# Optimization experiments

Hardware: AMD Instinct MI355X
Metric: run time of the kernel (lower is better)

The kernel has to match this reference:

```python
import jax, jax.numpy as jnp
import numpy as np

N = 4096  # square [B, T+1] as required by original indexing (T = shape[0], indexed on dim 1)
GAMMA = 0.99

def setup_inputs() -> dict:
    key = jax.random.key(0)
    ks = jax.random.split(key, 6)
    shape = (N, N)
    names = ["Q", "expected_target_Q", "target_Q", "rewards",
             "target_policy_probs", "behaviour_policy_probs"]
    return {n: jax.random.normal(k, shape, dtype=jnp.float32) for n, k in zip(names, ks)}

def _retrace_loss(Q, expected_target_Q, target_Q, rewards,
                  target_policy_probs, behaviour_policy_probs):
    rewards = rewards * 100.0
    # retrace weights c_t = exp(min(log pi - log b, 0)) = min(1, pi/b)
    c_ret = jnp.exp(jnp.minimum(target_policy_probs - behaviour_policy_probs, 0.0))
    T = Q.shape[0]  # faithful to original (square inputs => equals time length)
    last = target_Q[:, T - 1]  # Q_ret[:, -1] = target_Q[:, -1]
    # reverse-time linear recurrence via a single scan:
    # Q_ret[t-1] = r[t-1] + gamma*c[t]*(Q_ret[t] - target_Q[t]) + gamma*E[t]
    xs = (rewards[:, :T - 1].T[::-1],          # [T-1, B], t-1 = T-2 .. 0
          c_ret[:, 1:T].T[::-1],               # c[t],  t = T-1 .. 1
          target_Q[:, 1:T].T[::-1],
          expected_target_Q[:, 1:T].T[::-1])

    def step(q_next, x):
        r, c, tq, eq = x
        q = r + GAMMA * c * (q_next - tq) + GAMMA * eq
        return q, q

    _, qs = jax.lax.scan(step, last, xs)       # qs: [T-1, B] for t = T-2 .. 0
    Q_ret = jnp.concatenate([qs[::-1].T, last[:, None]], axis=1)  # [B, T]
    Q_ret = jax.lax.stop_gradient(Q_ret)       # computed under torch.no_grad()
    return jnp.mean((Q - Q_ret) ** 2)

def reference(Q, expected_target_Q, target_Q, rewards,
              target_policy_probs, behaviour_policy_probs):
    return _retrace_loss(Q, expected_target_Q, target_Q, rewards,
                         target_policy_probs, behaviour_policy_probs)
```

## Files before the change

### kernel.cpp

```cpp
#include <hip/hip_runtime.h>


#define NROWS 4096
#define TLEN  4096
#define BLOCK 256
#define EPT   16

__global__ __launch_bounds__(BLOCK) void retrace_main(
    const float* __restrict__ Q,
    const float* __restrict__ eQ,
    const float* __restrict__ tQ,
    const float* __restrict__ rw,
    const float* __restrict__ tpp,
    const float* __restrict__ bpp,
    double* __restrict__ partials)
{
    constexpr float G = 0.99f;
    __shared__ float sA[BLOCK];
    __shared__ float sB[BLOCK];
    __shared__ float sRed[BLOCK / 64];

    const int tid = threadIdx.x;
    const long long base = (long long)blockIdx.x * TLEN;
    const int ua = (TLEN - EPT) - EPT * tid;

    float Aa[17], Bb[17];

    float prev_r = 0.0f;
    #pragma unroll
    for (int g = 0; g < 4; ++g) {
        const float4 r4 = *(const float4*)(rw  + base + ua + 4 * g);
        const float4 t4 = *(const float4*)(tpp + base + ua + 4 * g);
        const float4 p4 = *(const float4*)(bpp + base + ua + 4 * g);
        const float4 q4 = *(const float4*)(tQ  + base + ua + 4 * g);
        const float4 e4 = *(const float4*)(eQ  + base + ua + 4 * g);
        const float rv[4] = {r4.x, r4.y, r4.z, r4.w};
        const float tv[4] = {t4.x, t4.y, t4.z, t4.w};
        const float pv[4] = {p4.x, p4.y, p4.z, p4.w};
        const float qv[4] = {q4.x, q4.y, q4.z, q4.w};
        const float ev[4] = {e4.x, e4.y, e4.z, e4.w};
        #pragma unroll
        for (int e = 0; e < 4; ++e) {
            const int m = 4 * g + e;
            if (m >= 1) {
                const float c  = __expf(fminf(tv[e] - pv[e], 0.0f));
                const float gc = G * c;
                const float f  = fmaf(-gc, qv[e], G * ev[e]);
                const float rp = (e == 0) ? prev_r : rv[e - 1];
                Aa[m] = gc;
                Bb[m] = fmaf(100.0f, rp, f);
            }
        }
        prev_r = rv[3];
    }
    if (tid == 0) {
        Aa[16] = 0.0f;
        Bb[16] = tQ[base + TLEN - 1];
    } else {
        const float tx = tpp[base + ua + 16];
        const float px = bpp[base + ua + 16];
        const float qx = tQ [base + ua + 16];
        const float ex = eQ [base + ua + 16];
        const float c  = __expf(fminf(tx - px, 0.0f));
        const float gc = G * c;
        const float f  = fmaf(-gc, qx, G * ex);
        Aa[16] = gc;
        Bb[16] = fmaf(100.0f, prev_r, f);
    }

    float Ac = 1.0f, Bc = 0.0f;
    #pragma unroll
    for (int k = 0; k < EPT; ++k) {
        const int m = 16 - k;
        Bc = fmaf(Aa[m], Bc, Bb[m]);
        Ac = Aa[m] * Ac;
    }

    sA[tid] = Ac; sB[tid] = Bc;
    __syncthreads();
    #pragma unroll
    for (int off = 1; off < BLOCK; off <<= 1) {
        float a1 = 0.0f, b1 = 0.0f;
        const bool has = (tid >= off);
        if (has) { a1 = sA[tid - off]; b1 = sB[tid - off]; }
        const float a2 = sA[tid], b2 = sB[tid];
        __syncthreads();
        if (has) { sA[tid] = a2 * a1; sB[tid] = fmaf(a2, b1, b2); }
        __syncthreads();
    }
    float y = (tid == 0) ? 0.0f : sB[tid - 1];

    float qq[16];
    #pragma unroll
    for (int g = 0; g < 4; ++g) {
        const float4 Q4 = *(const float4*)(Q + base + ua + 4 * g);
        qq[4 * g + 0] = Q4.x; qq[4 * g + 1] = Q4.y;
        qq[4 * g + 2] = Q4.z; qq[4 * g + 3] = Q4.w;
    }
    float acc = 0.0f;
    #pragma unroll
    for (int k = 0; k < EPT; ++k) {
        const int m = 16 - k;
        y = fmaf(Aa[m], y, Bb[m]);
        const float d = qq[m - 1] - y;
        acc = fmaf(d, d, acc);
    }

    #pragma unroll
    for (int off = 32; off > 0; off >>= 1)
        acc += __shfl_down(acc, off, 64);
    if ((tid & 63) == 0) sRed[tid >> 6] = acc;
    __syncthreads();
    if (tid == 0) {
        const float s = sRed[0] + sRed[1] + sRed[2] + sRed[3];
        partials[blockIdx.x] = (double)s;
    }
}

__global__ __launch_bounds__(BLOCK) void retrace_finalize(
    const double* __restrict__ partials, float* __restrict__ out)
{
    __shared__ double sRed[BLOCK / 64];
    double s = 0.0;
    for (int i = threadIdx.x; i < NROWS; i += BLOCK) s += partials[i];
    #pragma unroll
    for (int off = 32; off > 0; off >>= 1)
        s += __shfl_down(s, off, 64);
    if ((threadIdx.x & 63) == 0) sRed[threadIdx.x >> 6] = s;
    __syncthreads();
    if (threadIdx.x == 0) {
        const double tot = sRed[0] + sRed[1] + sRed[2] + sRed[3];
        out[0] = (float)(tot / ((double)NROWS * (double)TLEN));
    }
}

extern "C" void kernel_launch(void* const* d_in, const int* in_sizes, int n_in,
                              void* d_out, int out_size, void* d_ws, size_t ws_size,
                              hipStream_t stream)
{
    const float* Q   = (const float*)d_in[0];
    const float* eQ  = (const float*)d_in[1];
    const float* tQ  = (const float*)d_in[2];
    const float* rw  = (const float*)d_in[3];
    const float* tpp = (const float*)d_in[4];
    const float* bpp = (const float*)d_in[5];
    double* partials = (double*)d_ws;

    retrace_main<<<NROWS, BLOCK, 0, stream>>>(Q, eQ, tQ, rw, tpp, bpp, partials);
    retrace_finalize<<<1, BLOCK, 0, stream>>>(partials, (float*)d_out);
}
```

Baseline: 345.1 us.

## Replace shared-memory block scan with wavefront shuffle scan and hoist all loads

```diff
diff --git a/kernel.cpp b/kernel.cpp
--- a/kernel.cpp
+++ b/kernel.cpp
@@ -16,100 +16,120 @@
     double* __restrict__ partials)
 {
     constexpr float G = 0.99f;
-    __shared__ float sA[BLOCK];
-    __shared__ float sB[BLOCK];
-    __shared__ float sRed[BLOCK / 64];
+    __shared__ float sWA[4], sWB[4];
+    __shared__ float sRed[4];
 
-    const int tid = threadIdx.x;
+    const int tid  = threadIdx.x;
+    const int lane = tid & 63;
+    const int wv   = tid >> 6;
     const long long base = (long long)blockIdx.x * TLEN;
     const int ua = (TLEN - EPT) - EPT * tid;
 
-    float Aa[17], Bb[17];
+    float4 Rv4[4], Tv4[4], Pv4[4], Qt4[4], Ev4[4], Qm4[4];
+    #pragma unroll
+    for (int g = 0; g < 4; ++g) Rv4[g] = *(const float4*)(rw  + base + ua + 4 * g);
+    #pragma unroll
+    for (int g = 0; g < 4; ++g) Tv4[g] = *(const float4*)(tpp + base + ua + 4 * g);
+    #pragma unroll
+    for (int g = 0; g < 4; ++g) Pv4[g] = *(const float4*)(bpp + base + ua + 4 * g);
+    #pragma unroll
+    for (int g = 0; g < 4; ++g) Qt4[g] = *(const float4*)(tQ  + base + ua + 4 * g);
+    #pragma unroll
+    for (int g = 0; g < 4; ++g) Ev4[g] = *(const float4*)(eQ  + base + ua + 4 * g);
+    #pragma unroll
+    for (int g = 0; g < 4; ++g) Qm4[g] = *(const float4*)(Q   + base + ua + 4 * g);
 
-    float prev_r = 0.0f;
+    const bool bnd = (lane == 0) && (tid != 0);
+    float bt = 0.f, bp = 0.f, bq = 0.f, be = 0.f;
+    if (bnd) {
+        bt = tpp[base + ua + 16];
+        bp = bpp[base + ua + 16];
+        bq = tQ [base + ua + 16];
+        be = eQ [base + ua + 16];
+    }
+
+    float rv[16], tv[16], pv[16], qv[16], ev[16], qm[16];
     #pragma unroll
     for (int g = 0; g < 4; ++g) {
-        const float4 r4 = *(const float4*)(rw  + base + ua + 4 * g);
-        const float4 t4 = *(const float4*)(tpp + base + ua + 4 * g);
-        const float4 p4 = *(const float4*)(bpp + base + ua + 4 * g);
-        const float4 q4 = *(const float4*)(tQ  + base + ua + 4 * g);
-        const float4 e4 = *(const float4*)(eQ  + base + ua + 4 * g);
-        const float rv[4] = {r4.x, r4.y, r4.z, r4.w};
-        const float tv[4] = {t4.x, t4.y, t4.z, t4.w};
-        const float pv[4] = {p4.x, p4.y, p4.z, p4.w};
-        const float qv[4] = {q4.x, q4.y, q4.z, q4.w};
-        const float ev[4] = {e4.x, e4.y, e4.z, e4.w};
-        #pragma unroll
-        for (int e = 0; e < 4; ++e) {
-            const int m = 4 * g + e;
-            if (m >= 1) {
-                const float c  = __expf(fminf(tv[e] - pv[e], 0.0f));
-                const float gc = G * c;
-                const float f  = fmaf(-gc, qv[e], G * ev[e]);
-                const float rp = (e == 0) ? prev_r : rv[e - 1];
-                Aa[m] = gc;
-                Bb[m] = fmaf(100.0f, rp, f);
-            }
+        rv[4*g+0]=Rv4[g].x; rv[4*g+1]=Rv4[g].y; rv[4*g+2]=Rv4[g].z; rv[4*g+3]=Rv4[g].w;
+        tv[4*g+0]=Tv4[g].x; tv[4*g+1]=Tv4[g].y; tv[4*g+2]=Tv4[g].z; tv[4*g+3]=Tv4[g].w;
+        pv[4*g+0]=Pv4[g].x; pv[4*g+1]=Pv4[g].y; pv[4*g+2]=Pv4[g].z; pv[4*g+3]=Pv4[g].w;
+        qv[4*g+0]=Qt4[g].x; qv[4*g+1]=Qt4[g].y; qv[4*g+2]=Qt4[g].z; qv[4*g+3]=Qt4[g].w;
+        ev[4*g+0]=Ev4[g].x; ev[4*g+1]=Ev4[g].y; ev[4*g+2]=Ev4[g].z; ev[4*g+3]=Ev4[g].w;
+        qm[4*g+0]=Qm4[g].x; qm[4*g+1]=Qm4[g].y; qm[4*g+2]=Qm4[g].z; qm[4*g+3]=Qm4[g].w;
+    }
+
+    float Aa[16], Bb[16];
+    #pragma unroll
+    for (int m = 1; m <= 15; ++m) {
+        const float c  = __expf(fminf(tv[m] - pv[m], 0.0f));
+        const float gc = G * c;
+        const float f  = fmaf(-gc, qv[m], G * ev[m]);
+        Aa[m-1] = gc;
+        Bb[m-1] = fmaf(100.0f, rv[m-1], f);
+    }
+    {
+        float t16 = __shfl_up(tv[0], 1, 64);
+        float p16 = __shfl_up(pv[0], 1, 64);
+        float q16 = __shfl_up(qv[0], 1, 64);
+        float e16 = __shfl_up(ev[0], 1, 64);
+        if (bnd) { t16 = bt; p16 = bp; q16 = bq; e16 = be; }
+        if (tid == 0) {
+            Aa[15] = 0.0f;
+            Bb[15] = qv[15];
+        } else {
+            const float c  = __expf(fminf(t16 - p16, 0.0f));
+            const float gc = G * c;
+            const float f  = fmaf(-gc, q16, G * e16);
+            Aa[15] = gc;
+            Bb[15] = fmaf(100.0f, rv[15], f);
         }
-        prev_r = rv[3];
-    }
-    if (tid == 0) {
-        Aa[16] = 0.0f;
-        Bb[16] = tQ[base + TLEN - 1];
-    } else {
-        const float tx = tpp[base + ua + 16];
-        const float px = bpp[base + ua + 16];
-        const float qx = tQ [base + ua + 16];
-        const float ex = eQ [base + ua + 16];
-        const float c  = __expf(fminf(tx - px, 0.0f));
-        const float gc = G * c;
-        const float f  = fmaf(-gc, qx, G * ex);
-        Aa[16] = gc;
-        Bb[16] = fmaf(100.0f, prev_r, f);
     }
 
     float Ac = 1.0f, Bc = 0.0f;
     #pragma unroll
     for (int k = 0; k < EPT; ++k) {
-        const int m = 16 - k;
-        Bc = fmaf(Aa[m], Bc, Bb[m]);
-        Ac = Aa[m] * Ac;
+        const int idx = 15 - k;
+        Bc = fmaf(Aa[idx], Bc, Bb[idx]);
+        Ac = Aa[idx] * Ac;
     }
 
-    sA[tid] = Ac; sB[tid] = Bc;
+    float Ai = Ac, Bi = Bc;
+    #pragma unroll
+    for (int off = 1; off < 64; off <<= 1) {
+        const float Ap = __shfl_up(Ai, off, 64);
+        const float Bp = __shfl_up(Bi, off, 64);
+        if (lane >= off) {
+            Bi = fmaf(Ai, Bp, Bi);
+            Ai = Ai * Ap;
+        }
+    }
+
+    if (lane == 63) { sWA[wv] = Ai; sWB[wv] = Bi; }
     __syncthreads();
+    float Bp = 0.0f;
     #pragma unroll
-    for (int off = 1; off < BLOCK; off <<= 1) {
-        float a1 = 0.0f, b1 = 0.0f;
-        const bool has = (tid >= off);
-        if (has) { a1 = sA[tid - off]; b1 = sB[tid - off]; }
-        const float a2 = sA[tid], b2 = sB[tid];
-        __syncthreads();
-        if (has) { sA[tid] = a2 * a1; sB[tid] = fmaf(a2, b1, b2); }
-        __syncthreads();
-    }
-    float y = (tid == 0) ? 0.0f : sB[tid - 1];
+    for (int j = 0; j < 3; ++j)
+        if (j < wv) Bp = fmaf(sWA[j], Bp, sWB[j]);
 
-    float qq[16];
-    #pragma unroll
-    for (int g = 0; g < 4; ++g) {
-        const float4 Q4 = *(const float4*)(Q + base + ua + 4 * g);
-        qq[4 * g + 0] = Q4.x; qq[4 * g + 1] = Q4.y;
-        qq[4 * g + 2] = Q4.z; qq[4 * g + 3] = Q4.w;
-    }
+    float Ae = __shfl_up(Ai, 1, 64);
+    float Be = __shfl_up(Bi, 1, 64);
+    if (lane == 0) { Ae = 1.0f; Be = 0.0f; }
+    float y = fmaf(Ae, Bp, Be);
+
     float acc = 0.0f;
     #pragma unroll
     for (int k = 0; k < EPT; ++k) {
-        const int m = 16 - k;
-        y = fmaf(Aa[m], y, Bb[m]);
-        const float d = qq[m - 1] - y;
+        const int idx = 15 - k;
+        y = fmaf(Aa[idx], y, Bb[idx]);
+        const float d = qm[idx] - y;
         acc = fmaf(d, d, acc);
     }
 
     #pragma unroll
     for (int off = 32; off > 0; off >>= 1)
         acc += __shfl_down(acc, off, 64);
-    if ((tid & 63) == 0) sRed[tid >> 6] = acc;
+    if (lane == 0) sRed[wv] = acc;
     __syncthreads();
     if (tid == 0) {
         const float s = sRed[0] + sRed[1] + sRed[2] + sRed[3];
```

New measurement: 339.7 us. No clear change (-1.5%).
